# Kernel optimization log

Measured on AMD Instinct MI355X. Metric: run time of the kernel, lower is better.

## Reference

```python
import jax, jax.numpy as jnp
import numpy as np
from jax import lax

B, T, H = 16, 4096, 512

def setup_inputs() -> dict:
    key = jax.random.key(0)
    ks = jax.random.split(key, 10)
    return {
        "query": jax.random.normal(ks[0], (B, 1, H), dtype=jnp.float32),
        "value": jax.random.normal(ks[1], (B, T, H), dtype=jnp.float32),
        "last_attn": jax.random.uniform(ks[2], (B, T), dtype=jnp.float32),
        "conv_w": jax.random.normal(ks[3], (H, 1, 3), dtype=jnp.float32) * 0.05,
        "conv_b": jax.random.normal(ks[4], (H,), dtype=jnp.float32) * 0.05,
        "Wq": jax.random.normal(ks[5], (H, H), dtype=jnp.float32) * (1.0 / np.sqrt(H)),
        "Wv": jax.random.normal(ks[6], (H, H), dtype=jnp.float32) * (1.0 / np.sqrt(H)),
        "bias": jax.random.uniform(ks[7], (H,), minval=-0.1, maxval=0.1, dtype=jnp.float32),
        "w_score": jax.random.normal(ks[8], (1, H), dtype=jnp.float32) * (1.0 / np.sqrt(H)),
        "b_score": jax.random.normal(ks[9], (1,), dtype=jnp.float32) * 0.05,
    }

def reference(query, value, last_attn, conv_w, conv_b, Wq, Wv, bias, w_score, b_score):
    # conv1d over last_attn: (B,1,T) -> (B,H,T), kernel 3, pad 1
    conv = lax.conv_general_dilated(
        last_attn[:, None, :], conv_w, window_strides=(1,), padding="SAME",
        dimension_numbers=("NCH", "OIH", "NCH"))
    conv_attn = conv.transpose(0, 2, 1) + conv_b           # (B,T,H)
    q = jnp.einsum("bqh,oh->bqo", query, Wq)               # (B,1,H), Linear w/o bias: x @ W.T
    v = jnp.einsum("bth,oh->bto", value, Wv)               # (B,T,H)
    e = jnp.tanh(q + v + conv_attn + bias)                 # (B,T,H) broadcast over q_len=1
    score = jnp.einsum("bth,h->bt", e, w_score[0]) + b_score[0]  # (B,T)
    # smoothing=True: sigmoid + L1 normalize
    s = jax.nn.sigmoid(score)
    attn = s / jnp.sum(s, axis=-1, keepdims=True)          # (B,T)
    context = jnp.einsum("bt,bth->bh", attn, value)        # (B,H)
    out = jnp.concatenate([context, query[:, 0, :]], axis=1)  # (B,2H)
    return out, attn
```

## Files before the change

### kernel.cpp

```cpp
#include <hip/hip_runtime.h>
#include <hip/hip_bf16.h>
#include <cstddef>

#define BB 16
#define TT 4096
#define HH 512

typedef _Float16 half8 __attribute__((ext_vector_type(8)));
typedef float f32x4 __attribute__((ext_vector_type(4)));

__device__ __forceinline__ float fast_rcp(float x) { return __builtin_amdgcn_rcpf(x); }

__global__ void prep_kernel(const float* __restrict__ query,
                            const float* __restrict__ conv_b,
                            const float* __restrict__ Wq,
                            const float* __restrict__ Wv,
                            const float* __restrict__ bias,
                            _Float16* __restrict__ Bpack,
                            float* __restrict__ qb,
                            float* __restrict__ ssum,
                            float* __restrict__ ctx) {
    int blk = blockIdx.x;
    int tid = threadIdx.x;
    if (blk < 128) {
        int tn = blk >> 2, kq = blk & 3;
        int kb = kq * 4 + (tid >> 6);
        int lane = tid & 63;
        int n = tn * 16 + (lane & 15);
        int k = kb * 32 + ((lane >> 4) << 3);
        const float4* src = (const float4*)(Wv + (size_t)n * HH + k);
        float4 v0 = src[0], v1 = src[1];
        half8 h = { (_Float16)v0.x, (_Float16)v0.y, (_Float16)v0.z, (_Float16)v0.w,
                    (_Float16)v1.x, (_Float16)v1.y, (_Float16)v1.z, (_Float16)v1.w };
        *(half8*)(Bpack + ((size_t)(kb * 32 + tn) * 64 + lane) * 8) = h;
    } else if (blk < 192) {
        int q = blk - 128;
        int b = q >> 2, oq = q & 3;
        __shared__ float qrow[HH];
        for (int i = tid; i < HH; i += 256) qrow[i] = query[b * HH + i];
        __syncthreads();
        int wave = tid >> 6, lane = tid & 63;
        float4 q1 = *(const float4*)(qrow + lane * 8);
        float4 q2 = *(const float4*)(qrow + lane * 8 + 4);
        for (int i = wave; i < 128; i += 4) {
            int o = oq * 128 + i;
            const float4* w = (const float4*)(Wq + (size_t)o * HH);
            float4 a = w[lane * 2], c = w[lane * 2 + 1];
            float acc = a.x * q1.x + a.y * q1.y + a.z * q1.z + a.w * q1.w
                      + c.x * q2.x + c.y * q2.y + c.z * q2.z + c.w * q2.w;
            #pragma unroll
            for (int off = 1; off < 64; off <<= 1) acc += __shfl_xor(acc, off, 64);
            if (lane == 0) qb[b * HH + o] = acc + bias[o] + conv_b[o];
        }
    } else {
        for (int i = tid; i < BB; i += 256) ssum[i] = 0.f;
        for (int i = tid; i < BB * HH; i += 256) ctx[i] = 0.f;
    }
}

__global__ __launch_bounds__(512, 4) void gemm_fused_kernel(
        const float* __restrict__ value,
        const float* __restrict__ last_attn,
        const float* __restrict__ conv_w,
        const float* __restrict__ w_score,
        const float* __restrict__ b_score,
        const _Float16* __restrict__ Bpack,
        const float* __restrict__ qb,
        float* __restrict__ sbuf,
        float* __restrict__ ssum,
        float* __restrict__ ctx) {
    __shared__ _Float16 As[64 * 512];
    __shared__ float sred[64][8];
    __shared__ float s_lds[64];

    int tid = threadIdx.x;
    int blk = blockIdx.x;
    int b = blk >> 6;
    int t0 = (blk & 63) << 6;

    int lane = tid & 63, ng = tid >> 6;
    int quad = lane >> 4, lm = lane & 15;

    {
        int st = tid >> 3, cc = tid & 7;
        const float4* pA = (const float4*)(value + ((size_t)(b * TT + t0 + st)) * HH) + cc * 2;
        #pragma unroll
        for (int u = 0; u < 8; ++u) {
            float4 v0 = pA[u * 16], v1 = pA[u * 16 + 1];
            int cph = (cc + u * 8) ^ (st & 7);
            half8 h = { (_Float16)v0.x, (_Float16)v0.y, (_Float16)v0.z, (_Float16)v0.w,
                        (_Float16)v1.x, (_Float16)v1.y, (_Float16)v1.z, (_Float16)v1.w };
            *(half8*)(As + st * 512 + cph * 8) = h;
        }
    }

    f32x4 acc[4][4];
    #pragma unroll
    for (int mt = 0; mt < 4; ++mt)
        #pragma unroll
        for (int nt = 0; nt < 4; ++nt) { f32x4 z = {0.f,0.f,0.f,0.f}; acc[mt][nt] = z; }

    const _Float16* bp = Bpack + (size_t)(ng * 4) * 512 + lane * 8;
    half8 breg[2][4];
    #pragma unroll
    for (int nt = 0; nt < 4; ++nt)
        breg[0][nt] = *(const half8*)(bp + nt * 512);
    bp += 16384;

    __syncthreads();

    #pragma unroll 2
    for (int kb = 0; kb < 16; ++kb) {
        int cb = kb & 1;
        if (kb < 15) {
            #pragma unroll
            for (int nt = 0; nt < 4; ++nt)
                breg[cb ^ 1][nt] = *(const half8*)(bp + nt * 512);
            bp += 16384;
        }
        #pragma unroll
        for (int mt = 0; mt < 4; ++mt) {
            int tr = mt * 16 + lm;
            int cph = ((kb << 2) + quad) ^ (tr & 7);
            half8 a = *(const half8*)(As + tr * 512 + cph * 8);
            #pragma unroll
            for (int nt = 0; nt < 4; ++nt)
                acc[mt][nt] = __builtin_amdgcn_mfma_f32_16x16x32_f16(a, breg[cb][nt], acc[mt][nt], 0, 0, 0);
        }
    }

    float qvv[4], c0v[4], c1v[4], c2v[4], wvv[4];
    #pragma unroll
    for (int nt = 0; nt < 4; ++nt) {
        int o = ng * 64 + nt * 16 + lm;
        qvv[nt] = qb[b * HH + o];
        c0v[nt] = conv_w[o * 3 + 0];
        c1v[nt] = conv_w[o * 3 + 1];
        c2v[nt] = conv_w[o * 3 + 2];
        wvv[nt] = w_score[o];
    }
    float rs[4][4];
    #pragma unroll
    for (int mt = 0; mt < 4; ++mt) {
        #pragma unroll
        for (int j = 0; j < 4; ++j) {
            int tg = t0 + mt * 16 + quad * 4 + j;
            const float* la = last_attn + b * TT + tg;
            float lam = (tg > 0) ? la[-1] : 0.f;
            float la0 = la[0];
            float lap = (tg < TT - 1) ? la[1] : 0.f;
            float r = 0.f;
            #pragma unroll
            for (int nt = 0; nt < 4; ++nt) {
                float act = acc[mt][nt][j] + qvv[nt]
                          + c0v[nt] * lam + c1v[nt] * la0 + c2v[nt] * lap;
                act = fminf(15.f, fmaxf(-15.f, act));
                float e2 = __expf(2.f * act);
                r += (1.f - 2.f * fast_rcp(e2 + 1.f)) * wvv[nt];
            }
            rs[mt][j] = r;
        }
    }

    #pragma unroll
    for (int mt = 0; mt < 4; ++mt)
        #pragma unroll
        for (int j = 0; j < 4; ++j) {
            float v = rs[mt][j];
            #pragma unroll
            for (int off = 1; off < 16; off <<= 1) v += __shfl_xor(v, off, 64);
            if (lm == 0) sred[mt * 16 + quad * 4 + j][ng] = v;
        }
    __syncthreads();

    if (tid < 64) {
        float sc = b_score[0];
        #pragma unroll
        for (int k = 0; k < 8; ++k) sc += sred[tid][k];
        float s = fast_rcp(1.f + __expf(-sc));
        s_lds[tid] = s;
        sbuf[b * TT + t0 + tid] = s;
        float tot = s;
        #pragma unroll
        for (int off = 1; off < 64; off <<= 1) tot += __shfl_xor(tot, off, 64);
        if (tid == 0) atomicAdd(&ssum[b], tot);
    }
    __syncthreads();

    {
        int h = tid;
        int cl = h >> 3, j = h & 7;
        float a = 0.f;
        #pragma unroll 8
        for (int t2 = 0; t2 < 64; ++t2) {
            int cph = cl ^ (t2 & 7);
            a += s_lds[t2] * (float)As[t2 * 512 + cph * 8 + j];
        }
        atomicAdd(&ctx[b * HH + h], a);
    }
}

__global__ void finalize_kernel(const float* __restrict__ query,
                                const float* __restrict__ ctx,
                                const float* __restrict__ sbuf,
                                const float* __restrict__ ssum,
                                float* __restrict__ out) {
    int idx = blockIdx.x * 256 + threadIdx.x;
    if (idx < BB * 2 * HH) {
        int b = idx >> 10, c = idx & 1023;
        float v;
        if (c < HH) v = ctx[b * HH + c] / ssum[b];
        else        v = query[b * HH + (c - HH)];
        out[idx] = v;
    } else {
        int j = idx - BB * 2 * HH;
        int b = j >> 12, t = j & 4095;
        out[idx] = sbuf[b * TT + t] / ssum[b];
    }
}

extern "C" void kernel_launch(void* const* d_in, const int* in_sizes, int n_in,
                              void* d_out, int out_size, void* d_ws, size_t ws_size,
                              hipStream_t stream) {
    const float* query     = (const float*)d_in[0];
    const float* value     = (const float*)d_in[1];
    const float* last_attn = (const float*)d_in[2];
    const float* conv_w    = (const float*)d_in[3];
    const float* conv_b    = (const float*)d_in[4];
    const float* Wq        = (const float*)d_in[5];
    const float* Wv        = (const float*)d_in[6];
    const float* bias      = (const float*)d_in[7];
    const float* w_score   = (const float*)d_in[8];
    const float* b_score   = (const float*)d_in[9];

    char* ws = (char*)d_ws;
    _Float16* Bpack = (_Float16*)ws;
    float* qb     = (float*)(ws + 524288);
    float* sbuf   = (float*)(ws + 557056);
    float* ssum   = (float*)(ws + 819200);
    float* ctx    = (float*)(ws + 819264);
    float* out    = (float*)d_out;

    prep_kernel<<<193, 256, 0, stream>>>(query, conv_b, Wq, Wv, bias, Bpack, qb, ssum, ctx);
    gemm_fused_kernel<<<1024, 512, 0, stream>>>(value, last_attn, conv_w, w_score,
                                                b_score, Bpack, qb, sbuf, ssum, ctx);
    finalize_kernel<<<320, 256, 0, stream>>>(query, ctx, sbuf, ssum, out);
}
```

Measured before the change: 265.9 us.

## Double row tile to 128 timesteps per block with dynamic LDS

Each block now handles 128 timesteps instead of 64, so each wave covers 8 M-tiles and 2 N-tiles. This halves how often the packed Wv matrix is re-read per block and doubles reuse of each B fragment. The B-register prefetch is deepened to two k-steps ahead. The A tile now needs 128 KB of dynamic LDS, so occupancy drops to one block of 512 threads per CU, which reduces latency hiding for the global value loads.

```diff
diff --git a/kernel.cpp b/kernel.cpp
--- a/kernel.cpp
+++ b/kernel.cpp
@@ -58,7 +58,7 @@
     }
 }
 
-__global__ __launch_bounds__(512, 4) void gemm_fused_kernel(
+__global__ __launch_bounds__(512, 2) void gemm_fused_kernel(
         const float* __restrict__ value,
         const float* __restrict__ last_attn,
         const float* __restrict__ conv_w,
@@ -69,79 +69,85 @@
         float* __restrict__ sbuf,
         float* __restrict__ ssum,
         float* __restrict__ ctx) {
-    __shared__ _Float16 As[64 * 512];
-    __shared__ float sred[64][8];
-    __shared__ float s_lds[64];
+    extern __shared__ _Float16 As[];
+    __shared__ float sred[128][8];
+    __shared__ float s_lds[128];
 
     int tid = threadIdx.x;
     int blk = blockIdx.x;
-    int b = blk >> 6;
-    int t0 = (blk & 63) << 6;
+    int b = blk >> 5;
+    int t0 = (blk & 31) << 7;
 
     int lane = tid & 63, ng = tid >> 6;
     int quad = lane >> 4, lm = lane & 15;
 
+    const _Float16* bp = Bpack + (size_t)(ng * 2) * 512 + lane * 8;
+    half8 breg[4][2];
+    #pragma unroll
+    for (int kb = 0; kb < 2; ++kb)
+        #pragma unroll
+        for (int nt = 0; nt < 2; ++nt)
+            breg[kb][nt] = *(const half8*)(bp + kb * 16384 + nt * 512);
+    bp += 2 * 16384;
+
     {
         int st = tid >> 3, cc = tid & 7;
-        const float4* pA = (const float4*)(value + ((size_t)(b * TT + t0 + st)) * HH) + cc * 2;
-        #pragma unroll
-        for (int u = 0; u < 8; ++u) {
-            float4 v0 = pA[u * 16], v1 = pA[u * 16 + 1];
-            int cph = (cc + u * 8) ^ (st & 7);
-            half8 h = { (_Float16)v0.x, (_Float16)v0.y, (_Float16)v0.z, (_Float16)v0.w,
-                        (_Float16)v1.x, (_Float16)v1.y, (_Float16)v1.z, (_Float16)v1.w };
-            *(half8*)(As + st * 512 + cph * 8) = h;
-        }
-    }
-
-    f32x4 acc[4][4];
-    #pragma unroll
-    for (int mt = 0; mt < 4; ++mt)
-        #pragma unroll
-        for (int nt = 0; nt < 4; ++nt) { f32x4 z = {0.f,0.f,0.f,0.f}; acc[mt][nt] = z; }
-
-    const _Float16* bp = Bpack + (size_t)(ng * 4) * 512 + lane * 8;
-    half8 breg[2][4];
-    #pragma unroll
-    for (int nt = 0; nt < 4; ++nt)
-        breg[0][nt] = *(const half8*)(bp + nt * 512);
-    bp += 16384;
+        #pragma unroll
+        for (int r = 0; r < 2; ++r) {
+            int row = st + r * 64;
+            const float4* pA = (const float4*)(value + ((size_t)(b * TT + t0 + row)) * HH);
+            #pragma unroll
+            for (int u = 0; u < 8; ++u) {
+                int c_log = cc + u * 8;
+                float4 v0 = pA[2 * c_log], v1 = pA[2 * c_log + 1];
+                int cph = c_log ^ (row & 7);
+                half8 h = { (_Float16)v0.x, (_Float16)v0.y, (_Float16)v0.z, (_Float16)v0.w,
+                            (_Float16)v1.x, (_Float16)v1.y, (_Float16)v1.z, (_Float16)v1.w };
+                *(half8*)(As + row * 512 + cph * 8) = h;
+            }
+        }
+    }
+
+    f32x4 acc[8][2];
+    #pragma unroll
+    for (int mt = 0; mt < 8; ++mt)
+        #pragma unroll
+        for (int nt = 0; nt < 2; ++nt) { f32x4 z = {0.f,0.f,0.f,0.f}; acc[mt][nt] = z; }
 
     __syncthreads();
 
-    #pragma unroll 2
+    #pragma unroll 4
     for (int kb = 0; kb < 16; ++kb) {
-        int cb = kb & 1;
-        if (kb < 15) {
-            #pragma unroll
-            for (int nt = 0; nt < 4; ++nt)
-                breg[cb ^ 1][nt] = *(const half8*)(bp + nt * 512);
+        if (kb < 14) {
+            #pragma unroll
+            for (int nt = 0; nt < 2; ++nt)
+                breg[(kb + 2) & 3][nt] = *(const half8*)(bp + nt * 512);
             bp += 16384;
         }
         #pragma unroll
-        for (int mt = 0; mt < 4; ++mt) {
+        for (int mt = 0; mt < 8; ++mt) {
             int tr = mt * 16 + lm;
             int cph = ((kb << 2) + quad) ^ (tr & 7);
             half8 a = *(const half8*)(As + tr * 512 + cph * 8);
             #pragma unroll
-            for (int nt = 0; nt < 4; ++nt)
-                acc[mt][nt] = __builtin_amdgcn_mfma_f32_16x16x32_f16(a, breg[cb][nt], acc[mt][nt], 0, 0, 0);
-        }
-    }
-
-    float qvv[4], c0v[4], c1v[4], c2v[4], wvv[4];
-    #pragma unroll
-    for (int nt = 0; nt < 4; ++nt) {
-        int o = ng * 64 + nt * 16 + lm;
+            for (int nt = 0; nt < 2; ++nt)
+                acc[mt][nt] = __builtin_amdgcn_mfma_f32_16x16x32_f16(a, breg[kb & 3][nt], acc[mt][nt], 0, 0, 0);
+        }
+    }
+
+    float qvv[2], c0v[2], c1v[2], c2v[2], wvv[2];
+    #pragma unroll
+    for (int nt = 0; nt < 2; ++nt) {
+        int o = ng * 32 + nt * 16 + lm;
         qvv[nt] = qb[b * HH + o];
         c0v[nt] = conv_w[o * 3 + 0];
         c1v[nt] = conv_w[o * 3 + 1];
         c2v[nt] = conv_w[o * 3 + 2];
         wvv[nt] = w_score[o];
     }
-    float rs[4][4];
-    #pragma unroll
-    for (int mt = 0; mt < 4; ++mt) {
+    #pragma unroll
+    for (int mt = 0; mt < 8; ++mt) {
+        float rsj[4];
         #pragma unroll
         for (int j = 0; j < 4; ++j) {
             int tg = t0 + mt * 16 + quad * 4 + j;
@@ -151,29 +157,25 @@
             float lap = (tg < TT - 1) ? la[1] : 0.f;
             float r = 0.f;
             #pragma unroll
-            for (int nt = 0; nt < 4; ++nt) {
+            for (int nt = 0; nt < 2; ++nt) {
                 float act = acc[mt][nt][j] + qvv[nt]
                           + c0v[nt] * lam + c1v[nt] * la0 + c2v[nt] * lap;
                 act = fminf(15.f, fmaxf(-15.f, act));
                 float e2 = __expf(2.f * act);
                 r += (1.f - 2.f * fast_rcp(e2 + 1.f)) * wvv[nt];
             }
-            rs[mt][j] = r;
-        }
-    }
-
-    #pragma unroll
-    for (int mt = 0; mt < 4; ++mt)
-        #pragma unroll
-        for (int j = 0; j < 4; ++j) {
-            float v = rs[mt][j];
-            #pragma unroll
-            for (int off = 1; off < 16; off <<= 1) v += __shfl_xor(v, off, 64);
-            if (lm == 0) sred[mt * 16 + quad * 4 + j][ng] = v;
-        }
+            #pragma unroll
+            for (int off = 1; off < 16; off <<= 1) r += __shfl_xor(r, off, 64);
+            rsj[j] = r;
+        }
+        if (lm == 0)
+            #pragma unroll
+            for (int j = 0; j < 4; ++j)
+                sred[mt * 16 + quad * 4 + j][ng] = rsj[j];
+    }
     __syncthreads();
 
-    if (tid < 64) {
+    if (tid < 128) {
         float sc = b_score[0];
         #pragma unroll
         for (int k = 0; k < 8; ++k) sc += sred[tid][k];
@@ -183,7 +185,7 @@
         float tot = s;
         #pragma unroll
         for (int off = 1; off < 64; off <<= 1) tot += __shfl_xor(tot, off, 64);
-        if (tid == 0) atomicAdd(&ssum[b], tot);
+        if ((tid & 63) == 0) atomicAdd(&ssum[b], tot);
     }
     __syncthreads();
 
@@ -192,7 +194,7 @@
         int cl = h >> 3, j = h & 7;
         float a = 0.f;
         #pragma unroll 8
-        for (int t2 = 0; t2 < 64; ++t2) {
+        for (int t2 = 0; t2 < 128; ++t2) {
             int cph = cl ^ (t2 & 7);
             a += s_lds[t2] * (float)As[t2 * 512 + cph * 8 + j];
         }
@@ -241,8 +243,15 @@
     float* ctx    = (float*)(ws + 819264);
     float* out    = (float*)d_out;
 
+    static bool attr_set = false;
+    if (!attr_set) {
+        hipFuncSetAttribute((const void*)gemm_fused_kernel,
+                            hipFuncAttributeMaxDynamicSharedMemorySize, 131072);
+        attr_set = true;
+    }
+
     prep_kernel<<<193, 256, 0, stream>>>(query, conv_b, Wq, Wv, bias, Bpack, qb, ssum, ctx);
-    gemm_fused_kernel<<<1024, 512, 0, stream>>>(value, last_attn, conv_w, w_score,
-                                                b_score, Bpack, qb, sbuf, ssum, ctx);
+    gemm_fused_kernel<<<512, 512, 131072, stream>>>(value, last_attn, conv_w, w_score,
+                                                    b_score, Bpack, qb, sbuf, ssum, ctx);
     finalize_kernel<<<320, 256, 0, stream>>>(query, ctx, sbuf, ssum, out);
 }
```

New measurement: 259.9 us. -2.3%, faster.
